# Kernel optimization log

Hardware: AMD Instinct MI355X
Metric: run time of the kernel (lower is better)

The kernel has to match this reference:

```python
import jax, jax.numpy as jnp
import numpy as np

Na, Ns, Nb, Ne, MAXLEN, D = 16, 64, 100, 12, 20, 512
EPS = 1e-5
DELTA = 0.2
VIS_LAM = 1.0


def _make_boxes(key, shape):
    u = jax.random.uniform(key, shape + (4,), dtype=jnp.float32)
    xy = u[..., :2] * 0.7
    wh = u[..., 2:] * 0.3 + 0.01
    return jnp.concatenate([xy, xy + wh], axis=-1)  # valid xyxy boxes


def setup_inputs() -> dict:
    key = jax.random.key(0)
    k1, k2, k3, k4, k5 = jax.random.split(key, 5)
    return {
        "vis_feats": jax.random.normal(k1, (Na * Ns * Nb, D), dtype=jnp.float32),
        "word_feats": jax.random.normal(k2, (Na * Ne, D), dtype=jnp.float32),
        "boxes": _make_boxes(k3, (Na, Ns, Nb)),
        "detect_boxes": _make_boxes(k4, (Na, MAXLEN)),
        "entities_length": jax.random.randint(k5, (Na,), 0, Ne, dtype=jnp.int32),
    }


def _iou(a, b):
    # a, b: broadcastable (..., 4) xyxy. Same math as DVSA.IOU, vectorized.
    iw = jnp.minimum(a[..., 2], b[..., 2]) - jnp.maximum(a[..., 0], b[..., 0])
    ih = jnp.minimum(a[..., 3], b[..., 3]) - jnp.maximum(a[..., 1], b[..., 1])
    pos = (iw > 0) & (ih > 0)
    inter = jnp.where(pos, iw * ih, 0.0)
    a1 = (a[..., 2] - a[..., 0]) * (a[..., 3] - a[..., 1])
    a2 = (b[..., 2] - b[..., 0]) * (b[..., 3] - b[..., 1])
    denom = a1 + a2 - inter
    return jnp.where(pos, inter / jnp.where(denom > 0, denom, 1.0), 0.0)


def reference(vis_feats, word_feats, boxes, detect_boxes, entities_length):
    ar = jnp.arange(Na)
    div_vec = jnp.maximum(entities_length, 1).astype(vis_feats.dtype)          # zero2one
    word_mask = jnp.arange(Ne)[None, :] >= entities_length[:, None]            # (Na, Ne) True = padded entity

    # Ragged-masked similarity: (Na*Ns*Nb, Na*Ne)
    S_ = vis_feats @ word_feats.T
    S_ = jnp.where(word_mask.reshape(-1)[None, :], 0.0, S_)

    # Pairwise box IoU table (Na, Ns, Nb, MAXLEN) -- vectorized quadruple loop
    d_ti_n = _iou(boxes[:, :, :, None, :], detect_boxes[:, None, None, :, :])

    # --- visual consistency loss (train phase) ---
    S5 = S_.reshape(Na, Ns, Nb, Na, Ne)
    S_vis = S5[ar, :, :, ar, :]                                                # (Na, Ns, Nb, Ne) diagonal video<->caption
    sim_scr = jnp.max(S_vis, axis=2)                                           # (Na, Ns, Ne)
    maxind = jnp.argmax(S_vis, axis=2)                                         # best box per (video, seg, entity)
    flat_ind = (ar[:, None, None] * Ns + jnp.arange(Ns)[None, :, None]) * Nb + maxind
    mn = sim_scr.min(axis=1, keepdims=True)
    mx = sim_scr.max(axis=1, keepdims=True)
    sim_scr = jax.lax.stop_gradient((sim_scr - mn) / (mx - mn + EPS))[..., None]
    flat_ind = jax.lax.stop_gradient(flat_ind)

    v = vis_feats[flat_ind.reshape(-1)].reshape(Na, Ns, Ne, D)
    v = v / (jnp.linalg.norm(v, axis=3, keepdims=True) + EPS) * sim_scr
    v1 = v.transpose(0, 2, 1, 3).reshape(Na * Ne, Ns, D)
    gram = 1.0 - jnp.einsum('bsd,btd->bst', v1, v1).reshape(Na, Ne, Ns, Ns)
    eye = jnp.eye(Ns, dtype=bool)
    vis_mask = word_mask[:, :, None, None] | eye[None, None, :, :]
    gram = jnp.where(vis_mask, 0.0, gram)
    dem = jnp.maximum(jnp.count_nonzero(gram), 1).astype(gram.dtype)
    vis_loss = gram.sum() / dem

    # --- frame / margin score ---
    S = S_.reshape(Na * Ns, Nb, Na * Ne).max(axis=1).reshape(Na, Ns, Na * Ne)
    mn = S.min(axis=1, keepdims=True)
    mx = S.max(axis=1, keepdims=True)
    S = S * (S - mn) / (mx - mn + EPS)
    Sf = S.reshape(Na, Ns, Na, Ne).sum(axis=-1) / div_vec[None, None, :]        # (Na, Ns, Na)
    Sf_diag = Sf[ar, :, ar]                                                     # (Na, Ns)
    term1 = jax.nn.relu(Sf - Sf_diag.T[None, :, :] + DELTA).mean(axis=0).T      # (Na, Ns)
    term2 = jax.nn.relu(Sf - Sf_diag[:, :, None] + DELTA).mean(axis=2)          # (Na, Ns)
    frame_score = term1 + term2
    margin_loss = (frame_score.mean() + VIS_LAM * vis_loss) * 10.0

    S_sim = S_.reshape(Na * Ns, Nb, Na * Ne)
    D_sim = S_sim.max(axis=1)
    D_ind = S_sim.argmax(axis=1)
    return (D_ind, D_sim, margin_loss, d_ti_n)
```

## Files before the change

### kernel.cpp

```cpp
#include <hip/hip_runtime.h>
#include <math.h>

#define NA 16
#define NS 64
#define NB 100
#define NE 12
#define ML 20
#define DD 512
#define NC (NA*NE)
#define NR (NA*NS)
#define EPSF 1e-5f
#define DELTA_F 0.2f
#define IOU_TOTAL (NA*NS*NB*ML)
#define IOU_BLOCKS ((IOU_TOTAL + 255)/256)
#define MID_BLOCKS (NA*(NE+1))

#define ABUF 3328
#define BBUF 4096
#define TBUF (ABUF + BBUF)

__device__ inline void wave_minmax64(float v, float& mn, float& mx){
  mn = v; mx = v;
  #pragma unroll
  for (int off = 32; off > 0; off >>= 1){
    mn = fminf(mn, __shfl_xor(mn, off));
    mx = fmaxf(mx, __shfl_xor(mx, off));
  }
}

__device__ inline float block_sum256(float v, float* sred){
  int t = threadIdx.x;
  #pragma unroll
  for (int off = 32; off > 0; off >>= 1) v += __shfl_xor(v, off);
  if ((t & 63) == 0) sred[t >> 6] = v;
  __syncthreads();
  float tot = sred[0] + sred[1] + sred[2] + sred[3];
  __syncthreads();
  return tot;
}

__device__ __forceinline__ void wait_vmcnt(int n){
  switch (n){
    case 0: asm volatile("s_waitcnt vmcnt(0)" ::: "memory"); break;
    case 1: asm volatile("s_waitcnt vmcnt(1)" ::: "memory"); break;
    case 2: asm volatile("s_waitcnt vmcnt(2)" ::: "memory"); break;
    case 3: asm volatile("s_waitcnt vmcnt(3)" ::: "memory"); break;
    case 4: asm volatile("s_waitcnt vmcnt(4)" ::: "memory"); break;
    case 5: asm volatile("s_waitcnt vmcnt(5)" ::: "memory"); break;
    case 6: asm volatile("s_waitcnt vmcnt(6)" ::: "memory"); break;
    case 7: asm volatile("s_waitcnt vmcnt(7)" ::: "memory"); break;
    default: asm volatile("s_waitcnt vmcnt(8)" ::: "memory"); break;
  }
}

#define GLOAD_LDS(gp, lp) \
  __builtin_amdgcn_global_load_lds( \
      (const __attribute__((address_space(1))) void*)(gp), \
      (__attribute__((address_space(3))) void*)(lp), 16, 0, 0)

template<int JC>
__device__ __forceinline__ void gemm_pass(
    const float* __restrict__ abase, const float* __restrict__ word,
    const int* __restrict__ scols, float (*Tile)[TBUF],
    int t, int tc, int tb)
{
  constexpr int NL = 13 + 2*JC;
  constexpr int NSLOT = (NL + 3) >> 2;
  const int l = t & 63, w4 = t >> 6;
  const int sub = l >> 3, q = l & 7;

  int goff[NSLOT]; int ldso[NSLOT];
  #pragma unroll
  for (int s = 0; s < NSLOT; ++s){
    int L = w4 + 4*s;
    goff[s] = 0; ldso[s] = 0;
    if (L < NL){
      if (L < 13){
        int rb = L*8 + sub;
        int rbs = rb < NB ? rb : NB-1;
        goff[s] = rbs*DD + ((q ^ (rb & 7)) << 2);
        ldso[s] = L * 256;
      } else {
        int cb = (L-13)*8 + sub;
        goff[s] = scols[cb]*DD + ((q ^ (cb & 7)) << 2);
        ldso[s] = ABUF + (L-13) * 256;
      }
    }
  }
  const int nown = (NL - w4 + 3) >> 2;

  float acc[7][JC];
  #pragma unroll
  for (int j = 0; j < 7; ++j)
    #pragma unroll
    for (int jc = 0; jc < JC; ++jc) acc[j][jc] = 0.f;

  #pragma unroll
  for (int s = 0; s < NSLOT; ++s){
    int L = w4 + 4*s;
    if (L < NL){
      const float* g = (L < 13 ? abase : word) + goff[s];
      GLOAD_LDS(g, &Tile[0][ldso[s]]);
    }
  }

  int cur = 0;
  const int tcx = tc & 7;
  for (int k0 = 0; k0 < DD; k0 += 32){
    if (k0 + 32 < DD){
      #pragma unroll
      for (int s = 0; s < NSLOT; ++s){
        int L = w4 + 4*s;
        if (L < NL){
          const float* g = (L < 13 ? abase : word) + goff[s] + (k0 + 32);
          GLOAD_LDS(g, &Tile[cur^1][ldso[s]]);
        }
      }
      wait_vmcnt(nown);
    } else {
      wait_vmcnt(0);
    }
    __builtin_amdgcn_sched_barrier(0);
    __builtin_amdgcn_s_barrier();
    __builtin_amdgcn_sched_barrier(0);

    const float* As = &Tile[cur][0];
    const float* Bs = &Tile[cur][ABUF];
    #pragma unroll 4
    for (int kk = 0; kk < 32; kk += 2){
      const int j = kk >> 2, r2 = kk & 3;
      float2 breg[JC], areg[7];
      #pragma unroll
      for (int jc = 0; jc < JC; ++jc)
        breg[jc] = *(const float2*)&Bs[(jc*16 + tc)*32 + ((j ^ tcx) << 2) + r2];
      #pragma unroll
      for (int jj = 0; jj < 7; ++jj){
        int b = tb*7 + jj; b = (b < NB) ? b : (NB-1);
        areg[jj] = *(const float2*)&As[b*32 + ((j ^ (b & 7)) << 2) + r2];
      }
      #pragma unroll
      for (int jj = 0; jj < 7; ++jj)
        #pragma unroll
        for (int jc = 0; jc < JC; ++jc){
          float s0 = acc[jj][jc];
          s0 = fmaf(areg[jj].x, breg[jc].x, s0);
          s0 = fmaf(areg[jj].y, breg[jc].y, s0);
          acc[jj][jc] = s0;
        }
    }
    __builtin_amdgcn_sched_barrier(0);
    __builtin_amdgcn_s_barrier();
    cur ^= 1;
  }

  float* redv = &Tile[0][0];
  float* redi = &Tile[0][ABUF];
  #pragma unroll
  for (int jc = 0; jc < JC; ++jc){
    int ci = jc * 16 + tc;
    float best = -3.4e38f; int bi = 0;
    #pragma unroll
    for (int jj = 0; jj < 7; ++jj){
      int b = tb * 7 + jj;
      if (b < NB){ float v = acc[jj][jc]; if (v > best){ best = v; bi = b; } }
    }
    redv[ci * 16 + tb] = best;
    redi[ci * 16 + tb] = (float)bi;
  }
}

__device__ __forceinline__ void gemm_epilogue(
    const float* __restrict__ redv, const float* __restrict__ redi,
    const int* __restrict__ scols, int base, int ncols, int kcnt,
    float* __restrict__ dsim, float* __restrict__ dind, int r, int t)
{
  __syncthreads();
  if (t < ncols){
    int gi = base + t;
    if (gi < kcnt){
      float best = -3.4e38f; int bi = 0;
      #pragma unroll
      for (int g = 0; g < 16; ++g){
        float v = redv[t * 16 + g];
        if (v > best){ best = v; bi = (int)redi[t * 16 + g]; }
      }
      int c = scols[gi];
      dsim[r * NC + c] = best;
      dind[r * NC + c] = (float)bi;
    }
  }
  __syncthreads();
}

__global__ __launch_bounds__(256) void k_main(
    const float* __restrict__ vis, const float* __restrict__ word,
    const int* __restrict__ elen, const float* __restrict__ boxes,
    const float* __restrict__ det,
    float* __restrict__ dind, float* __restrict__ dsim, float* __restrict__ dtin,
    float* __restrict__ accums, unsigned int* __restrict__ done)
{
  const int t = threadIdx.x;

  if (blockIdx.x >= NR){
    int idx = (int)(blockIdx.x - NR) * 256 + t;
    if (idx < IOU_TOTAL){
      int m = idx % ML; int t2 = idx / ML; int b = t2 % NB; int t3 = t2 / NB;
      const float4 A = *(const float4*)(boxes + (size_t)(t3 * NB + b) * 4);
      int a = t3 / NS;
      const float4 B = *(const float4*)(det + (size_t)(a * ML + m) * 4);
      float iw = fminf(A.z, B.z) - fmaxf(A.x, B.x);
      float ih = fminf(A.w, B.w) - fmaxf(A.y, B.y);
      bool pos = (iw > 0.f) && (ih > 0.f);
      float inter = pos ? iw * ih : 0.f;
      float a1 = (A.z - A.x) * (A.w - A.y);
      float a2 = (B.z - B.x) * (B.w - B.y);
      float den = a1 + a2 - inter;
      dtin[idx] = pos ? inter / (den > 0.f ? den : 1.f) : 0.f;
    }
    return;
  }

  __shared__ float Tile[2][TBUF];
  __shared__ int   scols[NC];
  __shared__ int   s_el[NA];
  __shared__ int   s_cnt;
  const int r  = blockIdx.x;
  const int tc = t & 15;
  const int tb = t >> 4;

  if (r == 0 && t == 0){ accums[0] = 0.f; accums[1] = 0.f; done[0] = 0u; }

  if (t < NA){ int L = elen[t]; L = L < 0 ? 0 : (L > NE ? NE : L); s_el[t] = L; }
  if (t < NC){ dsim[r * NC + t] = 0.f; dind[r * NC + t] = 0.f; }
  __syncthreads();
  if (t < NC){
    int aw = t / NE, e = t - aw * NE;
    int base = 0;
    #pragma unroll
    for (int i = 0; i < NA; ++i) base += (i < aw) ? s_el[i] : 0;
    if (e < s_el[aw]) scols[base + e] = t;
  }
  if (t == 0){
    int n = 0;
    #pragma unroll
    for (int i = 0; i < NA; ++i) n += s_el[i];
    s_cnt = n;
  }
  __syncthreads();
  const int kcnt = s_cnt;
  if (t < NC && t >= kcnt) scols[t] = (kcnt > 0) ? scols[kcnt - 1] : 0;
  __syncthreads();

  const int jcnt = (kcnt + 15) >> 4;
  if (jcnt == 0) return;
  const float* abase = vis + (size_t)r * NB * DD;

  const int jc1 = (jcnt > 8) ? 8 : jcnt;
  switch (jc1){
    case 1: gemm_pass<1>(abase, word, scols, Tile, t, tc, tb); break;
    case 2: gemm_pass<2>(abase, word, scols, Tile, t, tc, tb); break;
    case 3: gemm_pass<3>(abase, word, scols, Tile, t, tc, tb); break;
    case 4: gemm_pass<4>(abase, word, scols, Tile, t, tc, tb); break;
    case 5: gemm_pass<5>(abase, word, scols, Tile, t, tc, tb); break;
    case 6: gemm_pass<6>(abase, word, scols, Tile, t, tc, tb); break;
    case 7: gemm_pass<7>(abase, word, scols, Tile, t, tc, tb); break;
    default: gemm_pass<8>(abase, word, scols, Tile, t, tc, tb); break;
  }
  gemm_epilogue(&Tile[0][0], &Tile[0][ABUF], scols, 0, jc1 * 16, kcnt, dsim, dind, r, t);

  if (jcnt > 8){
    const int jc2 = jcnt - 8;
    switch (jc2){
      case 1: gemm_pass<1>(abase, word, scols + 128, Tile, t, tc, tb); break;
      case 2: gemm_pass<2>(abase, word, scols + 128, Tile, t, tc, tb); break;
      default: gemm_pass<3>(abase, word, scols + 128, Tile, t, tc, tb); break;
    }
    gemm_epilogue(&Tile[0][0], &Tile[0][ABUF], scols, 128, jc2 * 16, kcnt, dsim, dind, r, t);
  }
}

__global__ __launch_bounds__(256) void k_mid(
    const float* __restrict__ vis, const float* __restrict__ dind,
    const float* __restrict__ dsim, const int* __restrict__ elen,
    float* __restrict__ sf, float* __restrict__ accums,
    unsigned int* __restrict__ done, float* __restrict__ out)
{
  const int a = blockIdx.x, y = blockIdx.y;
  const int t = threadIdx.x, lane = t & 63, w = t >> 6;
  __shared__ float sred[4];
  __shared__ int   s_mi[NS];
  __shared__ float s_inv[NS];
  __shared__ float s_nw2[NS];
  __shared__ float s_sn[NS];
  __shared__ int   s_last;

  if (y == NE){
    for (int aw = w; aw < NA; aw += 4){
      float accv = 0.f;
      for (int e = 0; e < NE; ++e){
        int c = aw * NE + e;
        float v = dsim[(a * NS + lane) * NC + c];
        float mn, mx; wave_minmax64(v, mn, mx);
        accv += v * (v - mn) / (mx - mn + EPSF);
      }
      float dv = fmaxf((float)elen[aw], 1.f);
      sf[(a * NS + lane) * NA + aw] = accv / dv;
    }
  } else {
    const int e = y;
    if (e < elen[a]){
      if (w == 0){
        float v = dsim[(a * NS + lane) * NC + (a * NE + e)];
        float mn, mx; wave_minmax64(v, mn, mx);
        s_sn[lane] = (v - mn) / (mx - mn + EPSF);
      }
      if (t < NS) s_mi[t] = (int)dind[(size_t)(a * NS + t) * NC + (a * NE + e)];
      __syncthreads();

      for (int s = w; s < NS; s += 4){
        const float* row = vis + (size_t)((a * NS + s) * NB + s_mi[s]) * DD;
        float4 v0 = *(const float4*)(row + lane * 8);
        float4 v1 = *(const float4*)(row + lane * 8 + 4);
        float ss = v0.x*v0.x + v0.y*v0.y + v0.z*v0.z + v0.w*v0.w
                 + v1.x*v1.x + v1.y*v1.y + v1.z*v1.z + v1.w*v1.w;
        #pragma unroll
        for (int off = 32; off > 0; off >>= 1) ss += __shfl_xor(ss, off);
        if (lane == 0){
          float sn = s_sn[s];
          float d = sqrtf(ss) + EPSF;
          s_inv[s] = sn / d;
          s_nw2[s] = sn * sn * ss / (d * d);
        }
      }
      __syncthreads();

      float W0 = 0.f, W1 = 0.f;
      #pragma unroll 8
      for (int s = 0; s < NS; ++s){
        const float* row = vis + (size_t)((a * NS + s) * NB + s_mi[s]) * DD;
        float inv = s_inv[s];
        W0 = fmaf(row[t],       inv, W0);
        W1 = fmaf(row[t + 256], inv, W1);
      }
      float w2  = block_sum256(W0 * W0 + W1 * W1, sred);
      float nw2 = block_sum256((t < NS) ? s_nw2[t] : 0.f, sred);
      if (t == 0){
        float part = (float)(NS * (NS - 1)) - w2 + nw2;
        atomicAdd(&accums[0], part);
        atomicAdd(&accums[1], (float)(NS * (NS - 1)));
      }
    }
  }

  __syncthreads();
  if (t == 0){
    __threadfence();
    unsigned int old = atomicAdd(done, 1u);
    s_last = (old == (unsigned int)(MID_BLOCKS - 1)) ? 1 : 0;
  }
  __syncthreads();
  if (s_last){
    __threadfence();
    float sum = 0.f;
    for (int i = t; i < NA * NS * NA; i += 256){
      int b = i & (NA - 1);
      int a2 = i >> 10;
      int s2 = (i >> 4) & (NS - 1);
      float v  = sf[i];
      float d1 = sf[(b * NS + s2) * NA + b];
      float d2 = sf[(a2 * NS + s2) * NA + a2];
      sum += fmaxf(v - d1 + DELTA_F, 0.f) + fmaxf(v - d2 + DELTA_F, 0.f);
    }
    float tot = block_sum256(sum, sred);
    if (t == 0){
      float frame = tot / (float)(NA * NA * NS);
      float cnt = accums[1];
      float vis_loss = accums[0] / fmaxf(cnt, 1.f);
      out[0] = (frame + vis_loss) * 10.f;
    }
  }
}

extern "C" void kernel_launch(void* const* d_in, const int* in_sizes, int n_in,
                              void* d_out, int out_size, void* d_ws, size_t ws_size,
                              hipStream_t stream)
{
  const float* vis   = (const float*)d_in[0];
  const float* word  = (const float*)d_in[1];
  const float* boxes = (const float*)d_in[2];
  const float* det   = (const float*)d_in[3];
  const int*   elen  = (const int*)d_in[4];

  float* out   = (float*)d_out;
  float* dind  = out;
  float* dsim  = out + NR * NC;
  float* mloss = out + 2 * NR * NC;
  float* dtin  = mloss + 1;

  float* ws     = (float*)d_ws;
  float* sf     = ws;
  float* accums = ws + NA * NS * NA;
  unsigned int* done = (unsigned int*)(accums + 2);

  k_main<<<NR + IOU_BLOCKS, 256, 0, stream>>>(vis, word, elen, boxes, det,
                                              dind, dsim, dtin, accums, done);
  k_mid<<<dim3(NA, NE + 1), 256, 0, stream>>>(vis, dind, dsim, elen,
                                              sf, accums, done, mloss);
}
```

Measured before the change: 440.1 us.

## Process two visual rows per block so word tiles are reused across rows

Each GEMM block now handles two (video,frame) rows, 200 boxes, against the selected word columns. When at most 96 columns are active it loads a doubled A tile and shares each loaded word tile across both rows. Wider column sets fall back to a per-row loop. This halves the GEMM block count from 1024 to 512 and cuts redundant word-feature loads, but it raises per-thread register use and LDS size and leaves fewer blocks to spread across CUs.

```diff
diff --git a/kernel.cpp b/kernel.cpp
--- a/kernel.cpp
+++ b/kernel.cpp
@@ -9,15 +9,18 @@
 #define DD 512
 #define NC (NA*NE)
 #define NR (NA*NS)
+#define NGB 512
 #define EPSF 1e-5f
 #define DELTA_F 0.2f
 #define IOU_TOTAL (NA*NS*NB*ML)
 #define IOU_BLOCKS ((IOU_TOTAL + 255)/256)
 #define MID_BLOCKS (NA*(NE+1))
 
-#define ABUF 3328
-#define BBUF 4096
-#define TBUF (ABUF + BBUF)
+#define ABUF2 6656
+#define BBUF2 3072
+#define TBUF2 (ABUF2 + BBUF2)
+#define ABUF1 3328
+#define BBUF1 4096
 
 __device__ inline void wave_minmax64(float v, float& mn, float& mx){
   mn = v; mx = v;
@@ -41,15 +44,19 @@
 
 __device__ __forceinline__ void wait_vmcnt(int n){
   switch (n){
-    case 0: asm volatile("s_waitcnt vmcnt(0)" ::: "memory"); break;
-    case 1: asm volatile("s_waitcnt vmcnt(1)" ::: "memory"); break;
-    case 2: asm volatile("s_waitcnt vmcnt(2)" ::: "memory"); break;
-    case 3: asm volatile("s_waitcnt vmcnt(3)" ::: "memory"); break;
-    case 4: asm volatile("s_waitcnt vmcnt(4)" ::: "memory"); break;
-    case 5: asm volatile("s_waitcnt vmcnt(5)" ::: "memory"); break;
-    case 6: asm volatile("s_waitcnt vmcnt(6)" ::: "memory"); break;
-    case 7: asm volatile("s_waitcnt vmcnt(7)" ::: "memory"); break;
-    default: asm volatile("s_waitcnt vmcnt(8)" ::: "memory"); break;
+    case 0:  asm volatile("s_waitcnt vmcnt(0)"  ::: "memory"); break;
+    case 1:  asm volatile("s_waitcnt vmcnt(1)"  ::: "memory"); break;
+    case 2:  asm volatile("s_waitcnt vmcnt(2)"  ::: "memory"); break;
+    case 3:  asm volatile("s_waitcnt vmcnt(3)"  ::: "memory"); break;
+    case 4:  asm volatile("s_waitcnt vmcnt(4)"  ::: "memory"); break;
+    case 5:  asm volatile("s_waitcnt vmcnt(5)"  ::: "memory"); break;
+    case 6:  asm volatile("s_waitcnt vmcnt(6)"  ::: "memory"); break;
+    case 7:  asm volatile("s_waitcnt vmcnt(7)"  ::: "memory"); break;
+    case 8:  asm volatile("s_waitcnt vmcnt(8)"  ::: "memory"); break;
+    case 9:  asm volatile("s_waitcnt vmcnt(9)"  ::: "memory"); break;
+    case 10: asm volatile("s_waitcnt vmcnt(10)" ::: "memory"); break;
+    case 11: asm volatile("s_waitcnt vmcnt(11)" ::: "memory"); break;
+    default: asm volatile("s_waitcnt vmcnt(12)" ::: "memory"); break;
   }
 }
 
@@ -58,22 +65,168 @@
       (const __attribute__((address_space(1))) void*)(gp), \
       (__attribute__((address_space(3))) void*)(lp), 16, 0, 0)
 
+#define PIPE_BARRIER() do { \
+  __builtin_amdgcn_sched_barrier(0); \
+  __builtin_amdgcn_s_barrier(); \
+  __builtin_amdgcn_sched_barrier(0); } while(0)
+
 template<int JC>
-__device__ __forceinline__ void gemm_pass(
+__device__ __forceinline__ void gemm2_pass(
+    const float* __restrict__ abase,
+    const float* __restrict__ word,
+    const int* __restrict__ scols, float (*Tile)[TBUF2],
+    int t, int tc, int tb)
+{
+  constexpr int NLA = 26;
+  constexpr int NL  = NLA + 2*JC;
+  constexpr int NSLOT = (NL + 3) >> 2;
+  const int w4 = t >> 6, l = t & 63;
+  const int sub = l >> 3, q = l & 7;
+
+  int goff[NSLOT], ldso[NSLOT];
+  #pragma unroll
+  for (int s = 0; s < NSLOT; ++s){
+    int L = w4 + 4*s; goff[s] = 0; ldso[s] = 0;
+    if (L < NL){
+      if (L < NLA){
+        int rr = L*8 + sub;
+        int rs = rr < 200 ? rr : 199;
+        goff[s] = rs*DD + ((q ^ (rr & 7)) << 2);
+        ldso[s] = L * 256;
+      } else {
+        int cb = (L - NLA)*8 + sub;
+        goff[s] = scols[cb]*DD + ((q ^ (cb & 7)) << 2);
+        ldso[s] = ABUF2 + (L - NLA) * 256;
+      }
+    }
+  }
+  const int nown = (NL - w4 + 3) >> 2;
+
+  float acc[2][7][JC];
+  #pragma unroll
+  for (int p = 0; p < 2; ++p)
+    #pragma unroll
+    for (int j = 0; j < 7; ++j)
+      #pragma unroll
+      for (int jc = 0; jc < JC; ++jc) acc[p][j][jc] = 0.f;
+
+  #pragma unroll
+  for (int s = 0; s < NSLOT; ++s){
+    int L = w4 + 4*s;
+    if (L < NL){
+      const float* g = (L < NLA ? abase : word) + goff[s];
+      GLOAD_LDS(g, &Tile[0][ldso[s]]);
+    }
+  }
+
+  int cur = 0;
+  const int tcx = tc & 7;
+  for (int k0 = 0; k0 < DD; k0 += 32){
+    if (k0 + 32 < DD){
+      #pragma unroll
+      for (int s = 0; s < NSLOT; ++s){
+        int L = w4 + 4*s;
+        if (L < NL){
+          const float* g = (L < NLA ? abase : word) + goff[s] + (k0 + 32);
+          GLOAD_LDS(g, &Tile[cur^1][ldso[s]]);
+        }
+      }
+      wait_vmcnt(nown);
+    } else {
+      wait_vmcnt(0);
+    }
+    PIPE_BARRIER();
+
+    const float* As = &Tile[cur][0];
+    const float* Bs = &Tile[cur][ABUF2];
+    #pragma unroll 4
+    for (int kk = 0; kk < 32; kk += 2){
+      const int j = kk >> 2, r2 = kk & 3;
+      float2 breg[JC], areg[2][7];
+      #pragma unroll
+      for (int jc = 0; jc < JC; ++jc)
+        breg[jc] = *(const float2*)&Bs[(jc*16 + tc)*32 + ((j ^ tcx) << 2) + r2];
+      #pragma unroll
+      for (int p = 0; p < 2; ++p)
+        #pragma unroll
+        for (int jj = 0; jj < 7; ++jj){
+          int b = tb*7 + jj; b = (b < NB) ? b : (NB-1);
+          int rr = p*100 + b;
+          areg[p][jj] = *(const float2*)&As[rr*32 + ((j ^ (rr & 7)) << 2) + r2];
+        }
+      #pragma unroll
+      for (int p = 0; p < 2; ++p)
+        #pragma unroll
+        for (int jj = 0; jj < 7; ++jj)
+          #pragma unroll
+          for (int jc = 0; jc < JC; ++jc){
+            float s0 = acc[p][jj][jc];
+            s0 = fmaf(areg[p][jj].x, breg[jc].x, s0);
+            s0 = fmaf(areg[p][jj].y, breg[jc].y, s0);
+            acc[p][jj][jc] = s0;
+          }
+    }
+    __builtin_amdgcn_sched_barrier(0);
+    __builtin_amdgcn_s_barrier();
+    cur ^= 1;
+  }
+
+  float* redv = &Tile[0][0];
+  float* redi = &Tile[0][ABUF2];
+  #pragma unroll
+  for (int p = 0; p < 2; ++p)
+    #pragma unroll
+    for (int jc = 0; jc < JC; ++jc){
+      int ci = jc * 16 + tc;
+      float best = -3.4e38f; int bi = 0;
+      #pragma unroll
+      for (int jj = 0; jj < 7; ++jj){
+        int b = tb * 7 + jj;
+        if (b < NB){ float v = acc[p][jj][jc]; if (v > best){ best = v; bi = b; } }
+      }
+      redv[p*1536 + ci*16 + tb] = best;
+      redi[p*1536 + ci*16 + tb] = (float)bi;
+    }
+}
+
+__device__ __forceinline__ void gemm2_epilogue(
+    const float* __restrict__ redv, const float* __restrict__ redi,
+    const int* __restrict__ scols, int kcnt,
+    float* __restrict__ dsim, float* __restrict__ dind, int r0, int t)
+{
+  __syncthreads();
+  if (t < kcnt){
+    int c = scols[t];
+    #pragma unroll
+    for (int p = 0; p < 2; ++p){
+      float best = -3.4e38f; int bi = 0;
+      #pragma unroll
+      for (int g = 0; g < 16; ++g){
+        float v = redv[p*1536 + t*16 + g];
+        if (v > best){ best = v; bi = (int)redi[p*1536 + t*16 + g]; }
+      }
+      dsim[(r0+p) * NC + c] = best;
+      dind[(r0+p) * NC + c] = (float)bi;
+    }
+  }
+  __syncthreads();
+}
+
+template<int JC>
+__device__ __forceinline__ void gemm1_pass(
     const float* __restrict__ abase, const float* __restrict__ word,
-    const int* __restrict__ scols, float (*Tile)[TBUF],
+    const int* __restrict__ scols, float (*Tile)[TBUF2],
     int t, int tc, int tb)
 {
   constexpr int NL = 13 + 2*JC;
   constexpr int NSLOT = (NL + 3) >> 2;
-  const int l = t & 63, w4 = t >> 6;
+  const int w4 = t >> 6, l = t & 63;
   const int sub = l >> 3, q = l & 7;
 
-  int goff[NSLOT]; int ldso[NSLOT];
+  int goff[NSLOT], ldso[NSLOT];
   #pragma unroll
   for (int s = 0; s < NSLOT; ++s){
-    int L = w4 + 4*s;
-    goff[s] = 0; ldso[s] = 0;
+    int L = w4 + 4*s; goff[s] = 0; ldso[s] = 0;
     if (L < NL){
       if (L < 13){
         int rb = L*8 + sub;
@@ -83,7 +236,7 @@
       } else {
         int cb = (L-13)*8 + sub;
         goff[s] = scols[cb]*DD + ((q ^ (cb & 7)) << 2);
-        ldso[s] = ABUF + (L-13) * 256;
+        ldso[s] = ABUF1 + (L-13) * 256;
       }
     }
   }
@@ -120,12 +273,10 @@
     } else {
       wait_vmcnt(0);
     }
-    __builtin_amdgcn_sched_barrier(0);
-    __builtin_amdgcn_s_barrier();
-    __builtin_amdgcn_sched_barrier(0);
+    PIPE_BARRIER();
 
     const float* As = &Tile[cur][0];
-    const float* Bs = &Tile[cur][ABUF];
+    const float* Bs = &Tile[cur][ABUF1];
     #pragma unroll 4
     for (int kk = 0; kk < 32; kk += 2){
       const int j = kk >> 2, r2 = kk & 3;
@@ -154,7 +305,7 @@
   }
 
   float* redv = &Tile[0][0];
-  float* redi = &Tile[0][ABUF];
+  float* redi = &Tile[0][ABUF1];
   #pragma unroll
   for (int jc = 0; jc < JC; ++jc){
     int ci = jc * 16 + tc;
@@ -169,7 +320,7 @@
   }
 }
 
-__device__ __forceinline__ void gemm_epilogue(
+__device__ __forceinline__ void gemm1_epilogue(
     const float* __restrict__ redv, const float* __restrict__ redi,
     const int* __restrict__ scols, int base, int ncols, int kcnt,
     float* __restrict__ dsim, float* __restrict__ dind, int r, int t)
@@ -201,8 +352,8 @@
 {
   const int t = threadIdx.x;
 
-  if (blockIdx.x >= NR){
-    int idx = (int)(blockIdx.x - NR) * 256 + t;
+  if (blockIdx.x >= NGB){
+    int idx = (int)(blockIdx.x - NGB) * 256 + t;
     if (idx < IOU_TOTAL){
       int m = idx % ML; int t2 = idx / ML; int b = t2 % NB; int t3 = t2 / NB;
       const float4 A = *(const float4*)(boxes + (size_t)(t3 * NB + b) * 4);
@@ -220,18 +371,21 @@
     return;
   }
 
-  __shared__ float Tile[2][TBUF];
+  __shared__ float Tile[2][TBUF2];
   __shared__ int   scols[NC];
   __shared__ int   s_el[NA];
   __shared__ int   s_cnt;
-  const int r  = blockIdx.x;
+  const int r0 = (int)blockIdx.x * 2;
   const int tc = t & 15;
   const int tb = t >> 4;
 
-  if (r == 0 && t == 0){ accums[0] = 0.f; accums[1] = 0.f; done[0] = 0u; }
+  if (blockIdx.x == 0 && t == 0){ accums[0] = 0.f; accums[1] = 0.f; done[0] = 0u; }
 
   if (t < NA){ int L = elen[t]; L = L < 0 ? 0 : (L > NE ? NE : L); s_el[t] = L; }
-  if (t < NC){ dsim[r * NC + t] = 0.f; dind[r * NC + t] = 0.f; }
+  if (t < NC){
+    dsim[r0 * NC + t] = 0.f;       dind[r0 * NC + t] = 0.f;
+    dsim[(r0+1) * NC + t] = 0.f;   dind[(r0+1) * NC + t] = 0.f;
+  }
   __syncthreads();
   if (t < NC){
     int aw = t / NE, e = t - aw * NE;
@@ -253,29 +407,38 @@
 
   const int jcnt = (kcnt + 15) >> 4;
   if (jcnt == 0) return;
-  const float* abase = vis + (size_t)r * NB * DD;
-
-  const int jc1 = (jcnt > 8) ? 8 : jcnt;
-  switch (jc1){
-    case 1: gemm_pass<1>(abase, word, scols, Tile, t, tc, tb); break;
-    case 2: gemm_pass<2>(abase, word, scols, Tile, t, tc, tb); break;
-    case 3: gemm_pass<3>(abase, word, scols, Tile, t, tc, tb); break;
-    case 4: gemm_pass<4>(abase, word, scols, Tile, t, tc, tb); break;
-    case 5: gemm_pass<5>(abase, word, scols, Tile, t, tc, tb); break;
-    case 6: gemm_pass<6>(abase, word, scols, Tile, t, tc, tb); break;
-    case 7: gemm_pass<7>(abase, word, scols, Tile, t, tc, tb); break;
-    default: gemm_pass<8>(abase, word, scols, Tile, t, tc, tb); break;
-  }
-  gemm_epilogue(&Tile[0][0], &Tile[0][ABUF], scols, 0, jc1 * 16, kcnt, dsim, dind, r, t);
-
-  if (jcnt > 8){
-    const int jc2 = jcnt - 8;
-    switch (jc2){
-      case 1: gemm_pass<1>(abase, word, scols + 128, Tile, t, tc, tb); break;
-      case 2: gemm_pass<2>(abase, word, scols + 128, Tile, t, tc, tb); break;
-      default: gemm_pass<3>(abase, word, scols + 128, Tile, t, tc, tb); break;
-    }
-    gemm_epilogue(&Tile[0][0], &Tile[0][ABUF], scols, 128, jc2 * 16, kcnt, dsim, dind, r, t);
+
+  if (jcnt <= 6){
+    const float* abase = vis + (size_t)r0 * NB * DD;
+    switch (jcnt){
+      case 1: gemm2_pass<1>(abase, word, scols, Tile, t, tc, tb); break;
+      case 2: gemm2_pass<2>(abase, word, scols, Tile, t, tc, tb); break;
+      case 3: gemm2_pass<3>(abase, word, scols, Tile, t, tc, tb); break;
+      case 4: gemm2_pass<4>(abase, word, scols, Tile, t, tc, tb); break;
+      case 5: gemm2_pass<5>(abase, word, scols, Tile, t, tc, tb); break;
+      default: gemm2_pass<6>(abase, word, scols, Tile, t, tc, tb); break;
+    }
+    gemm2_epilogue(&Tile[0][0], &Tile[0][ABUF2], scols, kcnt, dsim, dind, r0, t);
+  } else {
+    for (int p = 0; p < 2; ++p){
+      const float* abase = vis + (size_t)(r0 + p) * NB * DD;
+      const int jc1 = (jcnt > 8) ? 8 : jcnt;
+      if (jc1 == 7) gemm1_pass<7>(abase, word, scols, Tile, t, tc, tb);
+      else          gemm1_pass<8>(abase, word, scols, Tile, t, tc, tb);
+      gemm1_epilogue(&Tile[0][0], &Tile[0][ABUF1], scols, 0, jc1*16, kcnt,
+                     dsim, dind, r0 + p, t);
+      if (jcnt > 8){
+        const int jc2 = jcnt - 8;
+        switch (jc2){
+          case 1: gemm1_pass<1>(abase, word, scols + 128, Tile, t, tc, tb); break;
+          case 2: gemm1_pass<2>(abase, word, scols + 128, Tile, t, tc, tb); break;
+          case 3: gemm1_pass<3>(abase, word, scols + 128, Tile, t, tc, tb); break;
+          default: gemm1_pass<4>(abase, word, scols + 128, Tile, t, tc, tb); break;
+        }
+        gemm1_epilogue(&Tile[0][0], &Tile[0][ABUF1], scols, 128, jc2*16, kcnt,
+                       dsim, dind, r0 + p, t);
+      }
+    }
   }
 }
 
@@ -402,8 +565,8 @@
   float* accums = ws + NA * NS * NA;
   unsigned int* done = (unsigned int*)(accums + 2);
 
-  k_main<<<NR + IOU_BLOCKS, 256, 0, stream>>>(vis, word, elen, boxes, det,
-                                              dind, dsim, dtin, accums, done);
+  k_main<<<NGB + IOU_BLOCKS, 256, 0, stream>>>(vis, word, elen, boxes, det,
+                                               dind, dsim, dtin, accums, done);
   k_mid<<<dim3(NA, NE + 1), 256, 0, stream>>>(vis, dind, dsim, elen,
                                               sf, accums, done, mloss);
 }
```

Measured after the change: 520.7 us. +18.3%, slower.
